# Optimization experiments

Measured on AMD Instinct MI355X. Metric: run time of the kernel, lower is better.

Reference implementation:

```python
import jax, jax.numpy as jnp
import numpy as np

B, S, D, H = 2, 2048, 1024, 16
HD = D // H  # head_dim = 64


def setup_inputs() -> dict:
    key = jax.random.key(0)
    ks = jax.random.split(key, 12)
    s = 1.0 / np.sqrt(D)
    inp = {
        "query": jax.random.normal(ks[0], (B, S, D), jnp.float32),
        "key": jax.random.normal(ks[1], (B, S, D), jnp.float32),
        "value": jax.random.normal(ks[2], (B, S, D), jnp.float32),
        # causal mask, shape (B, S, S); 0 means masked
        "mask": jnp.broadcast_to(jnp.tril(jnp.ones((S, S), jnp.int32)), (B, S, S)),
        "Wq": jax.random.normal(ks[3], (D, D), jnp.float32) * s,
        "bq": jnp.zeros((D,), jnp.float32),
        "Wk": jax.random.normal(ks[4], (D, D), jnp.float32) * s,
        "bk": jnp.zeros((D,), jnp.float32),
        "Wv": jax.random.normal(ks[5], (D, D), jnp.float32) * s,
        "bv": jnp.zeros((D,), jnp.float32),
        "Wo": jax.random.normal(ks[6], (D, D), jnp.float32) * s,
        "bo": jnp.zeros((D,), jnp.float32),
    }
    return inp


def reference(query, key, value, mask, Wq, bq, Wk, bk, Wv, bv, Wo, bo):
    # QKV projections (nn.Linear: x @ W.T + b), split into heads -> (B, H, S, HD)
    def proj(x, W, b):
        return (x @ W.T + b).reshape(B, S, H, HD).transpose(0, 2, 1, 3)

    q = proj(query, Wq, bq)
    k = proj(key, Wk, bk)
    v = proj(value, Wv, bv)

    # scores: (B, H, S, S)
    scores = jnp.einsum("bhqd,bhkd->bhqk", q, k) / np.sqrt(HD).astype(np.float32)
    scores = jnp.where(mask[:, None, :, :] == 0, jnp.float32(-1e9), scores)
    attn = jax.nn.softmax(scores, axis=-1)
    # dropout is identity in eval mode
    ctx = jnp.einsum("bhqk,bhkd->bhqd", attn, v)  # (B, H, S, HD)
    ctx = ctx.transpose(0, 2, 1, 3).reshape(B, S, D)
    return ctx @ Wo.T + bo
```

## Files before the change

### kernel.cpp

```cpp
#include <hip/hip_runtime.h>
#include <hip/hip_bf16.h>
#include <stdint.h>


#define LOG2E 1.4426950408889634f

typedef __bf16 bf16x8 __attribute__((ext_vector_type(8)));
typedef float f32x4 __attribute__((ext_vector_type(4)));

__device__ __forceinline__ ushort f2bf(float f) {
  union { float f; uint32_t u; } v; v.f = f;
  uint32_t u = v.u + 0x7FFFu + ((v.u >> 16) & 1u);
  return (ushort)(u >> 16);
}
__device__ __forceinline__ uint32_t pack2(float a, float b) {
  return (uint32_t)f2bf(a) | ((uint32_t)f2bf(b) << 16);
}
__device__ __forceinline__ uint32_t pack2t(float a, float b) {
  uint32_t ua = __builtin_bit_cast(uint32_t, a);
  uint32_t ub = __builtin_bit_cast(uint32_t, b);
  return (ua >> 16) | (ub & 0xFFFF0000u);
}
__device__ __forceinline__ bf16x8 ld_frag(const ushort* p) {
  return __builtin_bit_cast(bf16x8, *(const uint4*)p);
}
__device__ __forceinline__ void gl_lds16(const void* g, void* l) {
  __builtin_amdgcn_global_load_lds(
      (const __attribute__((address_space(1))) void*)g,
      (__attribute__((address_space(3))) void*)l, 16, 0, 0);
}

template <int ROWS>
__device__ __forceinline__ void stage_tile(const ushort* src, int stride,
                                           ushort* dst, int wid, int lane) {
  const int rloc = lane >> 3;
  const int gsrc = (lane & 7) ^ (rloc & 7);
  constexpr int RW = ROWS / 4;
  const ushort* s = src + (size_t)(wid * RW + rloc) * stride + gsrc * 8;
#pragma unroll
  for (int j = 0; j < RW / 8; ++j)
    gl_lds16(s + (size_t)(j * 8) * stride, dst + (wid * RW + j * 8) * 64);
}
__device__ __forceinline__ int swz(int row, int gran) {
  return row * 64 + ((gran ^ (row & 7)) << 3);
}

__device__ __forceinline__ void cvt8(const float* s, ushort* d) {
  float4 f0 = ((const float4*)s)[0];
  float4 f1 = ((const float4*)s)[1];
  uint4 h;
  h.x = pack2(f0.x, f0.y); h.y = pack2(f0.z, f0.w);
  h.z = pack2(f1.x, f1.y); h.w = pack2(f1.z, f1.w);
  *(uint4*)d = h;
}

__global__ void cvt_all(const float* __restrict__ s0, const float* __restrict__ s1,
                        const float* __restrict__ s2, const float* __restrict__ s3,
                        const float* __restrict__ s4, const float* __restrict__ s5,
                        const float* __restrict__ s6, ushort* __restrict__ d0,
                        ushort* __restrict__ d1, ushort* __restrict__ d2,
                        ushort* __restrict__ d3, ushort* __restrict__ d4,
                        ushort* __restrict__ d5, ushort* __restrict__ d6) {
  int y = blockIdx.y;
  int n = (y < 3) ? (4096 * 1024) : (1024 * 1024);
  int i = (blockIdx.x * 256 + threadIdx.x) * 8;
  if (i >= n) return;
  const float* s; ushort* d;
  switch (y) {
    case 0: s = s0; d = d0; break;
    case 1: s = s1; d = d1; break;
    case 2: s = s2; d = d2; break;
    case 3: s = s3; d = d3; break;
    case 4: s = s4; d = d4; break;
    case 5: s = s5; d = d5; break;
    default: s = s6; d = d6; break;
  }
  cvt8(s + i, d + i);
}

template <int BN, bool OUT_BF16, bool PROJ3>
__global__ __launch_bounds__(256, 2) void gemm_bt(
    const ushort* __restrict__ A0, const ushort* __restrict__ A1, const ushort* __restrict__ A2,
    const ushort* __restrict__ W0, const ushort* __restrict__ W1, const ushort* __restrict__ W2,
    const float* __restrict__ b0, const float* __restrict__ b1, const float* __restrict__ b2,
    void* __restrict__ Y0, void* __restrict__ Y1, void* __restrict__ Y2,
    int Ndim, int Kdim) {
  __shared__ ushort Al[2][128 * 64];
  __shared__ ushort Bl[2][BN * 64];

  const int z = PROJ3 ? blockIdx.z : 0;
  const ushort* A = (z == 0) ? A0 : (z == 1) ? A1 : A2;
  const ushort* W = (z == 0) ? W0 : (z == 1) ? W1 : W2;
  const float* bias = (z == 0) ? b0 : (z == 1) ? b1 : b2;
  void* Yp = (z == 0) ? Y0 : (z == 1) ? Y1 : Y2;

  const int tid = threadIdx.x;
  const int wid = tid >> 6, lane = tid & 63;
  const int row0 = blockIdx.y * 128, col0 = blockIdx.x * BN;
  const int wr = wid >> 1, wc = wid & 1;
  const int lr = lane & 15, lg = lane >> 4;
  constexpr int NF = BN / 32;

  const ushort* Arow = A + (size_t)row0 * Kdim;
  const ushort* Wrow = W + (size_t)col0 * Kdim;

  f32x4 acc[4][NF] = {};

  stage_tile<128>(Arow, Kdim, Al[0], wid, lane);
  stage_tile<BN>(Wrow, Kdim, Bl[0], wid, lane);
  __syncthreads();

  int cur = 0;
  for (int k0 = 0; k0 < Kdim; k0 += 64) {
    if (k0 + 64 < Kdim) {
      stage_tile<128>(Arow + k0 + 64, Kdim, Al[cur ^ 1], wid, lane);
      stage_tile<BN>(Wrow + k0 + 64, Kdim, Bl[cur ^ 1], wid, lane);
    }
    const ushort* Ac = Al[cur];
    const ushort* Bc = Bl[cur];
#pragma unroll
    for (int kk = 0; kk < 2; ++kk) {
      bf16x8 af[4], bfr[NF];
#pragma unroll
      for (int m = 0; m < 4; ++m)
        af[m] = ld_frag(&Ac[swz(wr * 64 + m * 16 + lr, kk * 4 + lg)]);
#pragma unroll
      for (int n = 0; n < NF; ++n)
        bfr[n] = ld_frag(&Bc[swz(wc * (BN / 2) + n * 16 + lr, kk * 4 + lg)]);
#pragma unroll
      for (int m = 0; m < 4; ++m)
#pragma unroll
        for (int n = 0; n < NF; ++n)
          acc[m][n] = __builtin_amdgcn_mfma_f32_16x16x32_bf16(af[m], bfr[n], acc[m][n], 0, 0, 0);
    }
    __syncthreads();
    cur ^= 1;
  }

#pragma unroll
  for (int n = 0; n < NF; ++n) {
    int col = col0 + wc * (BN / 2) + n * 16 + lr;
    float bv = bias[col];
#pragma unroll
    for (int m = 0; m < 4; ++m) {
#pragma unroll
      for (int r = 0; r < 4; ++r) {
        int row = row0 + wr * 64 + m * 16 + lg * 4 + r;
        float v = acc[m][n][r] + bv;
        if (OUT_BF16)
          ((ushort*)Yp)[(size_t)row * Ndim + col] = f2bf(v);
        else
          ((float*)Yp)[(size_t)row * Ndim + col] = v;
      }
    }
  }
}

__global__ __launch_bounds__(256, 2) void attn_kernel(
    const ushort* __restrict__ Qb, const ushort* __restrict__ Kb,
    const ushort* __restrict__ Vb, ushort* __restrict__ Cx) {
  __shared__ ushort Kl[2][64 * 64];
  __shared__ ushort Vt[64 * 64];
  __shared__ ushort Pl[4][16 * 64];

  const int tid = threadIdx.x;
  const int wid = tid >> 6, lane = tid & 63;
  const int lr = lane & 15, lg = lane >> 4;
  const int x = blockIdx.x;
  const int p = blockIdx.y;
  const int b = x >> 4, h = x & 15;
  const size_t base = (size_t)b * 2048 * 1024 + h * 64;
  const float SCL = 0.125f * LOG2E;
  const int vp = tid & 31;
  const int vc = tid >> 5;

#pragma unroll 1
  for (int seg = 0; seg < 2; ++seg) {
    const int qi = seg ? (31 - p) : p;
    const int qb0 = qi * 64;
    const int q0w = qb0 + wid * 16;
    const int nt = qi + 1;

    bf16x8 qf[2];
    {
      const ushort* qs = Qb + base + (size_t)(q0w + lr) * 1024 + lg * 8;
      qf[0] = ld_frag(qs);
      qf[1] = ld_frag(qs + 32);
    }

    f32x4 O[4] = {};
    float m_reg = -1e30f, l_reg = 0.f;

    stage_tile<64>(Kb + base, 1024, Kl[0], wid, lane);
    uint4 va = *(const uint4*)(Vb + base + (size_t)(2 * vp) * 1024 + vc * 8);
    uint4 vb = *(const uint4*)(Vb + base + (size_t)(2 * vp + 1) * 1024 + vc * 8);

#pragma unroll 1
    for (int t = 0; t < nt; ++t) {
      const int kv0 = t * 64;
      {
        const ushort* pA = (const ushort*)&va;
        const ushort* pB = (const ushort*)&vb;
#pragma unroll
        for (int j = 0; j < 8; ++j) {
          int d = vc * 8 + j;
          int idx = d * 64 + (((vp >> 2) ^ j) << 3) + ((vp * 2) & 7);
          *(uint32_t*)&Vt[idx] = (uint32_t)pA[j] | ((uint32_t)pB[j] << 16);
        }
      }
      __syncthreads();

      if (t + 1 < nt) {
        stage_tile<64>(Kb + base + (size_t)(kv0 + 64) * 1024, 1024, Kl[(t + 1) & 1], wid, lane);
        va = *(const uint4*)(Vb + base + (size_t)(kv0 + 64 + 2 * vp) * 1024 + vc * 8);
        vb = *(const uint4*)(Vb + base + (size_t)(kv0 + 64 + 2 * vp + 1) * 1024 + vc * 8);
      }

      const bool dm = (t == nt - 1);
      const ushort* Kc = Kl[t & 1];

      f32x4 st[4];
#pragma unroll
      for (int cb = 0; cb < 4; ++cb) {
        if (kv0 + cb * 16 > q0w + 15) {
          st[cb] = f32x4{-1e30f, -1e30f, -1e30f, -1e30f};
          continue;
        }
        f32x4 a = {};
#pragma unroll
        for (int kk = 0; kk < 2; ++kk) {
          bf16x8 kfrag = ld_frag(&Kc[swz(cb * 16 + lr, kk * 4 + lg)]);
          a = __builtin_amdgcn_mfma_f32_16x16x32_bf16(kfrag, qf[kk], a, 0, 0, 0);
        }
#pragma unroll
        for (int r = 0; r < 4; ++r) {
          float s = a[r] * SCL;
          if (dm) {
            int kv = kv0 + cb * 16 + lg * 4 + r;
            if (kv > q0w + lr) s = -1e30f;
          }
          a[r] = s;
        }
        st[cb] = a;
      }

      float tmax = -1e30f;
#pragma unroll
      for (int cb = 0; cb < 4; ++cb) {
        float c01 = fmaxf(st[cb][0], st[cb][1]);
        float c23 = fmaxf(st[cb][2], st[cb][3]);
        tmax = fmaxf(tmax, fmaxf(c01, c23));
      }
      tmax = fmaxf(tmax, __shfl_xor(tmax, 16));
      tmax = fmaxf(tmax, __shfl_xor(tmax, 32));

      const bool skip = __all(tmax - m_reg <= 8.f);
      float mcur;
      if (skip) {
        mcur = m_reg;
      } else {
        mcur = fmaxf(m_reg, tmax);
        float alpha = exp2f(m_reg - mcur);
        m_reg = mcur;
        l_reg *= alpha;
        float aO[4];
#pragma unroll
        for (int r = 0; r < 4; ++r)
          aO[r] = __shfl(alpha, (lane & 48) | ((lane >> 2) & 12) | r);
#pragma unroll
        for (int n = 0; n < 4; ++n)
#pragma unroll
          for (int r = 0; r < 4; ++r) O[n][r] *= aO[r];
      }

      float ts = 0.f;
#pragma unroll
      for (int cb = 0; cb < 4; ++cb)
#pragma unroll
        for (int r = 0; r < 4; ++r) {
          float pv = exp2f(st[cb][r] - mcur);
          st[cb][r] = pv;
          ts += pv;
        }
      ts += __shfl_xor(ts, 16);
      ts += __shfl_xor(ts, 32);
      l_reg += ts;

      ushort* pw = &Pl[wid][0];
#pragma unroll
      for (int cb = 0; cb < 4; ++cb) {
        int g = ((cb * 2 + (lg >> 1)) ^ (lr & 7)) << 3;
        int idx = lr * 64 + g + ((lg & 1) * 4);
        *(uint32_t*)&pw[idx] = pack2t(st[cb][0], st[cb][1]);
        *(uint32_t*)&pw[idx + 2] = pack2t(st[cb][2], st[cb][3]);
      }

#pragma unroll
      for (int kk = 0; kk < 2; ++kk) {
        bf16x8 pa = ld_frag(&pw[swz(lr, kk * 4 + lg)]);
#pragma unroll
        for (int n = 0; n < 4; ++n) {
          bf16x8 vfr = ld_frag(&Vt[swz(n * 16 + lr, kk * 4 + lg)]);
          O[n] = __builtin_amdgcn_mfma_f32_16x16x32_bf16(pa, vfr, O[n], 0, 0, 0);
        }
      }
      __syncthreads();
    }

#pragma unroll
    for (int r = 0; r < 4; ++r) {
      float ls = __shfl(l_reg, (lane & 48) | ((lane >> 2) & 12) | r);
      float inv = 1.f / ls;
      size_t row = (size_t)b * 2048 + q0w + lg * 4 + r;
#pragma unroll
      for (int n = 0; n < 4; ++n)
        Cx[row * 1024 + h * 64 + n * 16 + lr] = f2bf(O[n][r] * inv);
    }
  }
}

extern "C" void kernel_launch(void* const* d_in, const int* in_sizes, int n_in,
                              void* d_out, int out_size, void* d_ws, size_t ws_size,
                              hipStream_t stream) {
  const float* query = (const float*)d_in[0];
  const float* key_i = (const float*)d_in[1];
  const float* value = (const float*)d_in[2];
  const float* Wq = (const float*)d_in[4];
  const float* bq = (const float*)d_in[5];
  const float* Wk = (const float*)d_in[6];
  const float* bk = (const float*)d_in[7];
  const float* Wv = (const float*)d_in[8];
  const float* bv = (const float*)d_in[9];
  const float* Wo = (const float*)d_in[10];
  const float* bo = (const float*)d_in[11];
  float* out = (float*)d_out;

  const size_t MD = (size_t)4096 * 1024;
  const size_t DD = (size_t)1024 * 1024;
  ushort* qbf = (ushort*)d_ws;
  ushort* kbf = qbf + MD;
  ushort* vbf = kbf + MD;
  ushort* Wqb = vbf + MD;
  ushort* Wkb = Wqb + DD;
  ushort* Wvb = Wkb + DD;
  ushort* Wob = Wvb + DD;
  ushort* Qb = Wob + DD;
  ushort* Kb = Qb + MD;
  ushort* Vb = Kb + MD;
  ushort* Cx = Vb + MD;

  cvt_all<<<dim3(2048, 7), 256, 0, stream>>>(query, key_i, value, Wq, Wk, Wv, Wo,
                                             qbf, kbf, vbf, Wqb, Wkb, Wvb, Wob);

  gemm_bt<128, true, true><<<dim3(8, 32, 3), 256, 0, stream>>>(
      qbf, kbf, vbf, Wqb, Wkb, Wvb, bq, bk, bv, Qb, Kb, Vb, 1024, 1024);

  attn_kernel<<<dim3(32, 16), 256, 0, stream>>>(Qb, Kb, Vb, Cx);

  gemm_bt<64, false, false><<<dim3(16, 32, 1), 256, 0, stream>>>(
      Cx, Cx, Cx, Wob, Wob, Wob, bo, bo, bo, out, out, out, 1024, 1024);
}
```

Before: 265.6 us.

## Fuse fp32-to-bf16 conversion into register-staged GEMMs and shrink attention blocks

Drops the separate conversion kernel. The GEMMs now load fp32 activations and weights directly, convert them to bf16 in registers and stage them into LDS with a register prefetch two tiles ahead. Block indices are remapped to group row tiles per XCD for L2 locality. The attention kernel moves to 128-thread blocks of 32 query rows with twice as many blocks, and some __syncthreads calls are replaced with explicit waitcnt plus s_barrier. Together these remove the conversion pass and its extra memory traffic, at the cost of more global fp32 reads per GEMM tile and halved attention K/V reuse per block.

After: 344.7 us. 29.8% more time.

```diff
diff --git a/kernel.cpp b/kernel.cpp
--- a/kernel.cpp
+++ b/kernel.cpp
@@ -4,6 +4,9 @@
 
 
 #define LOG2E 1.4426950408889634f
+#define LGKM0 asm volatile("s_waitcnt lgkmcnt(0)" ::: "memory")
+#define SCHED0 __builtin_amdgcn_sched_barrier(0)
+#define BAR __builtin_amdgcn_s_barrier()
 
 typedef __bf16 bf16x8 __attribute__((ext_vector_type(8)));
 typedef float f32x4 __attribute__((ext_vector_type(4)));
@@ -13,9 +16,6 @@
   uint32_t u = v.u + 0x7FFFu + ((v.u >> 16) & 1u);
   return (ushort)(u >> 16);
 }
-__device__ __forceinline__ uint32_t pack2(float a, float b) {
-  return (uint32_t)f2bf(a) | ((uint32_t)f2bf(b) << 16);
-}
 __device__ __forceinline__ uint32_t pack2t(float a, float b) {
   uint32_t ua = __builtin_bit_cast(uint32_t, a);
   uint32_t ub = __builtin_bit_cast(uint32_t, b);
@@ -30,100 +30,118 @@
       (__attribute__((address_space(3))) void*)l, 16, 0, 0);
 }
 
-template <int ROWS>
+__device__ __forceinline__ int swz(int row, int gran) {
+  return row * 64 + ((gran ^ (row & 7)) << 3);
+}
+
+template <int ROWS, int NW>
 __device__ __forceinline__ void stage_tile(const ushort* src, int stride,
                                            ushort* dst, int wid, int lane) {
   const int rloc = lane >> 3;
   const int gsrc = (lane & 7) ^ (rloc & 7);
-  constexpr int RW = ROWS / 4;
+  constexpr int RW = ROWS / NW;
   const ushort* s = src + (size_t)(wid * RW + rloc) * stride + gsrc * 8;
 #pragma unroll
   for (int j = 0; j < RW / 8; ++j)
     gl_lds16(s + (size_t)(j * 8) * stride, dst + (wid * RW + j * 8) * 64);
 }
-__device__ __forceinline__ int swz(int row, int gran) {
-  return row * 64 + ((gran ^ (row & 7)) << 3);
-}
-
-__device__ __forceinline__ void cvt8(const float* s, ushort* d) {
-  float4 f0 = ((const float4*)s)[0];
-  float4 f1 = ((const float4*)s)[1];
-  uint4 h;
-  h.x = pack2(f0.x, f0.y); h.y = pack2(f0.z, f0.w);
-  h.z = pack2(f1.x, f1.y); h.w = pack2(f1.z, f1.w);
-  *(uint4*)d = h;
-}
-
-__global__ void cvt_all(const float* __restrict__ s0, const float* __restrict__ s1,
-                        const float* __restrict__ s2, const float* __restrict__ s3,
-                        const float* __restrict__ s4, const float* __restrict__ s5,
-                        const float* __restrict__ s6, ushort* __restrict__ d0,
-                        ushort* __restrict__ d1, ushort* __restrict__ d2,
-                        ushort* __restrict__ d3, ushort* __restrict__ d4,
-                        ushort* __restrict__ d5, ushort* __restrict__ d6) {
-  int y = blockIdx.y;
-  int n = (y < 3) ? (4096 * 1024) : (1024 * 1024);
-  int i = (blockIdx.x * 256 + threadIdx.x) * 8;
-  if (i >= n) return;
-  const float* s; ushort* d;
-  switch (y) {
-    case 0: s = s0; d = d0; break;
-    case 1: s = s1; d = d1; break;
-    case 2: s = s2; d = d2; break;
-    case 3: s = s3; d = d3; break;
-    case 4: s = s4; d = d4; break;
-    case 5: s = s5; d = d5; break;
-    default: s = s6; d = d6; break;
-  }
-  cvt8(s + i, d + i);
-}
-
-template <int BN, bool OUT_BF16, bool PROJ3>
-__global__ __launch_bounds__(256, 2) void gemm_bt(
-    const ushort* __restrict__ A0, const ushort* __restrict__ A1, const ushort* __restrict__ A2,
-    const ushort* __restrict__ W0, const ushort* __restrict__ W1, const ushort* __restrict__ W2,
+
+template <int ROWS>
+struct StF32 {
+  static constexpr int TPR = 256 / ROWS, CPT = 64 / TPR, NL = CPT / 4, NG = CPT / 8;
+  float4 f[NL];
+  __device__ __forceinline__ void load(const float* base, int Kdim, int tid, int k0) {
+    const int row = tid / TPR, part = tid % TPR;
+    const float* p = base + (size_t)row * Kdim + k0 + part * CPT;
+#pragma unroll
+    for (int j = 0; j < NL; ++j) f[j] = ((const float4*)p)[j];
+  }
+  __device__ __forceinline__ void store(ushort* dst, int tid) {
+    const int row = tid / TPR, part = tid % TPR;
+#pragma unroll
+    for (int g = 0; g < NG; ++g) {
+      uint4 h;
+      h.x = pack2t(f[2 * g].x, f[2 * g].y);
+      h.y = pack2t(f[2 * g].z, f[2 * g].w);
+      h.z = pack2t(f[2 * g + 1].x, f[2 * g + 1].y);
+      h.w = pack2t(f[2 * g + 1].z, f[2 * g + 1].w);
+      *(uint4*)&dst[swz(row, part * NG + g)] = h;
+    }
+  }
+};
+template <int ROWS>
+struct StB16 {
+  static constexpr int TPR = 256 / ROWS, CPT = 64 / TPR, NG = CPT / 8;
+  uint4 u[NG];
+  __device__ __forceinline__ void load(const ushort* base, int Kdim, int tid, int k0) {
+    const int row = tid / TPR, part = tid % TPR;
+    const ushort* p = base + (size_t)row * Kdim + k0 + part * CPT;
+#pragma unroll
+    for (int g = 0; g < NG; ++g) u[g] = ((const uint4*)p)[g];
+  }
+  __device__ __forceinline__ void store(ushort* dst, int tid) {
+    const int row = tid / TPR, part = tid % TPR;
+#pragma unroll
+    for (int g = 0; g < NG; ++g) *(uint4*)&dst[swz(row, part * NG + g)] = u[g];
+  }
+};
+
+template <int BN, int NX, bool A_BF16, bool OUT_BF16, bool PROJ3>
+__global__ __launch_bounds__(256, 2) void gemm_rs(
+    const void* __restrict__ A0, const void* __restrict__ A1, const void* __restrict__ A2,
+    const float* __restrict__ W0, const float* __restrict__ W1, const float* __restrict__ W2,
     const float* __restrict__ b0, const float* __restrict__ b1, const float* __restrict__ b2,
     void* __restrict__ Y0, void* __restrict__ Y1, void* __restrict__ Y2,
     int Ndim, int Kdim) {
   __shared__ ushort Al[2][128 * 64];
   __shared__ ushort Bl[2][BN * 64];
 
-  const int z = PROJ3 ? blockIdx.z : 0;
-  const ushort* A = (z == 0) ? A0 : (z == 1) ? A1 : A2;
-  const ushort* W = (z == 0) ? W0 : (z == 1) ? W1 : W2;
+  const int z = PROJ3 ? blockIdx.y : 0;
+  const void* Ap = (z == 0) ? A0 : (z == 1) ? A1 : A2;
+  const float* W = (z == 0) ? W0 : (z == 1) ? W1 : W2;
   const float* bias = (z == 0) ? b0 : (z == 1) ? b1 : b2;
   void* Yp = (z == 0) ? Y0 : (z == 1) ? Y1 : Y2;
 
+  const int id = blockIdx.x;
+  const int xcd = id & 7;
+  const int slot = id >> 3;
+  const int by = xcd * 4 + (slot & 3);
+  const int bx = slot >> 2;
+
   const int tid = threadIdx.x;
   const int wid = tid >> 6, lane = tid & 63;
-  const int row0 = blockIdx.y * 128, col0 = blockIdx.x * BN;
+  const int row0 = by * 128, col0 = bx * BN;
   const int wr = wid >> 1, wc = wid & 1;
   const int lr = lane & 15, lg = lane >> 4;
   constexpr int NF = BN / 32;
 
-  const ushort* Arow = A + (size_t)row0 * Kdim;
-  const ushort* Wrow = W + (size_t)col0 * Kdim;
-
+  const float* Af = (const float*)Ap + (size_t)row0 * Kdim;
+  const ushort* Ab = (const ushort*)Ap + (size_t)row0 * Kdim;
+  const float* Wrow = W + (size_t)col0 * Kdim;
+
+  StF32<128> af32; StB16<128> ab16; StF32<BN> ws;
   f32x4 acc[4][NF] = {};
 
-  stage_tile<128>(Arow, Kdim, Al[0], wid, lane);
-  stage_tile<BN>(Wrow, Kdim, Bl[0], wid, lane);
-  __syncthreads();
-
+  if (A_BF16) { ab16.load(Ab, Kdim, tid, 0); } else { af32.load(Af, Kdim, tid, 0); }
+  ws.load(Wrow, Kdim, tid, 0);
+  if (A_BF16) { ab16.store(Al[0], tid); } else { af32.store(Al[0], tid); }
+  ws.store(Bl[0], tid);
+  if (A_BF16) { ab16.load(Ab, Kdim, tid, 64); } else { af32.load(Af, Kdim, tid, 64); }
+  ws.load(Wrow, Kdim, tid, 64);
+  LGKM0; SCHED0; BAR;
+
+  const int NT = Kdim >> 6;
   int cur = 0;
-  for (int k0 = 0; k0 < Kdim; k0 += 64) {
-    if (k0 + 64 < Kdim) {
-      stage_tile<128>(Arow + k0 + 64, Kdim, Al[cur ^ 1], wid, lane);
-      stage_tile<BN>(Wrow + k0 + 64, Kdim, Bl[cur ^ 1], wid, lane);
-    }
+#pragma unroll 1
+  for (int t = 0; t < NT; ++t) {
     const ushort* Ac = Al[cur];
     const ushort* Bc = Bl[cur];
 #pragma unroll
     for (int kk = 0; kk < 2; ++kk) {
-      bf16x8 af[4], bfr[NF];
+      bf16x8 afr[4], bfr[NF];
 #pragma unroll
       for (int m = 0; m < 4; ++m)
-        af[m] = ld_frag(&Ac[swz(wr * 64 + m * 16 + lr, kk * 4 + lg)]);
+        afr[m] = ld_frag(&Ac[swz(wr * 64 + m * 16 + lr, kk * 4 + lg)]);
 #pragma unroll
       for (int n = 0; n < NF; ++n)
         bfr[n] = ld_frag(&Bc[swz(wc * (BN / 2) + n * 16 + lr, kk * 4 + lg)]);
@@ -131,9 +149,18 @@
       for (int m = 0; m < 4; ++m)
 #pragma unroll
         for (int n = 0; n < NF; ++n)
-          acc[m][n] = __builtin_amdgcn_mfma_f32_16x16x32_bf16(af[m], bfr[n], acc[m][n], 0, 0, 0);
-    }
-    __syncthreads();
+          acc[m][n] = __builtin_amdgcn_mfma_f32_16x16x32_bf16(afr[m], bfr[n], acc[m][n], 0, 0, 0);
+    }
+    if (t + 1 < NT) {
+      if (A_BF16) { ab16.store(Al[cur ^ 1], tid); } else { af32.store(Al[cur ^ 1], tid); }
+      ws.store(Bl[cur ^ 1], tid);
+      if (t + 2 < NT) {
+        if (A_BF16) { ab16.load(Ab, Kdim, tid, (t + 2) * 64); }
+        else { af32.load(Af, Kdim, tid, (t + 2) * 64); }
+        ws.load(Wrow, Kdim, tid, (t + 2) * 64);
+      }
+    }
+    LGKM0; SCHED0; BAR;
     cur ^= 1;
   }
 
@@ -156,12 +183,12 @@
   }
 }
 
-__global__ __launch_bounds__(256, 2) void attn_kernel(
+__global__ __launch_bounds__(128, 2) void attn_kernel(
     const ushort* __restrict__ Qb, const ushort* __restrict__ Kb,
     const ushort* __restrict__ Vb, ushort* __restrict__ Cx) {
   __shared__ ushort Kl[2][64 * 64];
   __shared__ ushort Vt[64 * 64];
-  __shared__ ushort Pl[4][16 * 64];
+  __shared__ ushort Pl[2][16 * 64];
 
   const int tid = threadIdx.x;
   const int wid = tid >> 6, lane = tid & 63;
@@ -172,14 +199,14 @@
   const size_t base = (size_t)b * 2048 * 1024 + h * 64;
   const float SCL = 0.125f * LOG2E;
   const int vp = tid & 31;
-  const int vc = tid >> 5;
+  const int c0 = tid >> 5;
 
 #pragma unroll 1
   for (int seg = 0; seg < 2; ++seg) {
-    const int qi = seg ? (31 - p) : p;
-    const int qb0 = qi * 64;
+    const int qi = seg ? (63 - p) : p;
+    const int qb0 = qi * 32;
     const int q0w = qb0 + wid * 16;
-    const int nt = qi + 1;
+    const int nt = (qi >> 1) + 1;
 
     bf16x8 qf[2];
     {
@@ -191,29 +218,39 @@
     f32x4 O[4] = {};
     float m_reg = -1e30f, l_reg = 0.f;
 
-    stage_tile<64>(Kb + base, 1024, Kl[0], wid, lane);
-    uint4 va = *(const uint4*)(Vb + base + (size_t)(2 * vp) * 1024 + vc * 8);
-    uint4 vb = *(const uint4*)(Vb + base + (size_t)(2 * vp + 1) * 1024 + vc * 8);
+    stage_tile<64, 2>(Kb + base, 1024, Kl[0], wid, lane);
+    uint4 va0 = *(const uint4*)(Vb + base + (size_t)(2 * vp) * 1024 + c0 * 8);
+    uint4 vb0 = *(const uint4*)(Vb + base + (size_t)(2 * vp + 1) * 1024 + c0 * 8);
+    uint4 va1 = *(const uint4*)(Vb + base + (size_t)(2 * vp) * 1024 + (c0 + 4) * 8);
+    uint4 vb1 = *(const uint4*)(Vb + base + (size_t)(2 * vp + 1) * 1024 + (c0 + 4) * 8);
 
 #pragma unroll 1
     for (int t = 0; t < nt; ++t) {
       const int kv0 = t * 64;
       {
-        const ushort* pA = (const ushort*)&va;
-        const ushort* pB = (const ushort*)&vb;
+        const ushort* pA0 = (const ushort*)&va0;
+        const ushort* pB0 = (const ushort*)&vb0;
+        const ushort* pA1 = (const ushort*)&va1;
+        const ushort* pB1 = (const ushort*)&vb1;
 #pragma unroll
         for (int j = 0; j < 8; ++j) {
-          int d = vc * 8 + j;
-          int idx = d * 64 + (((vp >> 2) ^ j) << 3) + ((vp * 2) & 7);
-          *(uint32_t*)&Vt[idx] = (uint32_t)pA[j] | ((uint32_t)pB[j] << 16);
-        }
-      }
-      __syncthreads();
+          int idx = (c0 * 8 + j) * 64 + (((vp >> 2) ^ j) << 3) + ((vp * 2) & 7);
+          *(uint32_t*)&Vt[idx] = (uint32_t)pA0[j] | ((uint32_t)pB0[j] << 16);
+        }
+#pragma unroll
+        for (int j = 0; j < 8; ++j) {
+          int idx = ((c0 + 4) * 8 + j) * 64 + (((vp >> 2) ^ j) << 3) + ((vp * 2) & 7);
+          *(uint32_t*)&Vt[idx] = (uint32_t)pA1[j] | ((uint32_t)pB1[j] << 16);
+        }
+      }
+      LGKM0; SCHED0; BAR;
 
       if (t + 1 < nt) {
-        stage_tile<64>(Kb + base + (size_t)(kv0 + 64) * 1024, 1024, Kl[(t + 1) & 1], wid, lane);
-        va = *(const uint4*)(Vb + base + (size_t)(kv0 + 64 + 2 * vp) * 1024 + vc * 8);
-        vb = *(const uint4*)(Vb + base + (size_t)(kv0 + 64 + 2 * vp + 1) * 1024 + vc * 8);
+        stage_tile<64, 2>(Kb + base + (size_t)(kv0 + 64) * 1024, 1024, Kl[(t + 1) & 1], wid, lane);
+        va0 = *(const uint4*)(Vb + base + (size_t)(kv0 + 64 + 2 * vp) * 1024 + c0 * 8);
+        vb0 = *(const uint4*)(Vb + base + (size_t)(kv0 + 64 + 2 * vp + 1) * 1024 + c0 * 8);
+        va1 = *(const uint4*)(Vb + base + (size_t)(kv0 + 64 + 2 * vp) * 1024 + (c0 + 4) * 8);
+        vb1 = *(const uint4*)(Vb + base + (size_t)(kv0 + 64 + 2 * vp + 1) * 1024 + (c0 + 4) * 8);
       }
 
       const bool dm = (t == nt - 1);
@@ -234,12 +271,12 @@
         }
 #pragma unroll
         for (int r = 0; r < 4; ++r) {
-          float s = a[r] * SCL;
+          float sv = a[r] * SCL;
           if (dm) {
             int kv = kv0 + cb * 16 + lg * 4 + r;
-            if (kv > q0w + lr) s = -1e30f;
+            if (kv > q0w + lr) sv = -1e30f;
           }
-          a[r] = s;
+          a[r] = sv;
         }
         st[cb] = a;
       }
@@ -304,7 +341,7 @@
           O[n] = __builtin_amdgcn_mfma_f32_16x16x32_bf16(pa, vfr, O[n], 0, 0, 0);
         }
       }
-      __syncthreads();
+      BAR;
     }
 
 #pragma unroll
@@ -336,27 +373,16 @@
   float* out = (float*)d_out;
 
   const size_t MD = (size_t)4096 * 1024;
-  const size_t DD = (size_t)1024 * 1024;
-  ushort* qbf = (ushort*)d_ws;
-  ushort* kbf = qbf + MD;
-  ushort* vbf = kbf + MD;
-  ushort* Wqb = vbf + MD;
-  ushort* Wkb = Wqb + DD;
-  ushort* Wvb = Wkb + DD;
-  ushort* Wob = Wvb + DD;
-  ushort* Qb = Wob + DD;
+  ushort* Qb = (ushort*)d_ws;
   ushort* Kb = Qb + MD;
   ushort* Vb = Kb + MD;
   ushort* Cx = Vb + MD;
 
-  cvt_all<<<dim3(2048, 7), 256, 0, stream>>>(query, key_i, value, Wq, Wk, Wv, Wo,
-                                             qbf, kbf, vbf, Wqb, Wkb, Wvb, Wob);
-
-  gemm_bt<128, true, true><<<dim3(8, 32, 3), 256, 0, stream>>>(
-      qbf, kbf, vbf, Wqb, Wkb, Wvb, bq, bk, bv, Qb, Kb, Vb, 1024, 1024);
-
-  attn_kernel<<<dim3(32, 16), 256, 0, stream>>>(Qb, Kb, Vb, Cx);
-
-  gemm_bt<64, false, false><<<dim3(16, 32, 1), 256, 0, stream>>>(
-      Cx, Cx, Cx, Wob, Wob, Wob, bo, bo, bo, out, out, out, 1024, 1024);
-}
+  gemm_rs<128, 8, false, true, true><<<dim3(256, 3), 256, 0, stream>>>(
+      query, key_i, value, Wq, Wk, Wv, bq, bk, bv, Qb, Kb, Vb, 1024, 1024);
+
+  attn_kernel<<<dim3(32, 32), 128, 0, stream>>>(Qb, Kb, Vb, Cx);
+
+  gemm_rs<64, 16, true, false, false><<<dim3(512, 1), 256, 0, stream>>>(
+      Cx, Cx, Cx, Wo, Wo, Wo, bo, bo, bo, out, out, out, 1024, 1024);
+}
```
